# Kernel tuning notes

Hardware: AMD Instinct MI355X
Metric: run time of the kernel (lower is better)

The kernel has to match this reference:

```python
import jax, jax.numpy as jnp
import numpy as np

N, E, D, H = 50000, 800000, 64, 2
DH = D // H  # per-head GAT width
BN_EPS = 1e-5


def _linear_params(key, fan_in, fan_out):
    k1, k2 = jax.random.split(key)
    s = 1.0 / np.sqrt(fan_in)
    W = jax.random.uniform(k1, (fan_in, fan_out), jnp.float32, -s, s)
    b = jax.random.uniform(k2, (fan_out,), jnp.float32, -s, s)
    return W, b


def setup_inputs() -> dict:
    key = jax.random.key(0)
    ks = jax.random.split(key, 12)
    node_feats = jax.random.normal(ks[0], (N, D), jnp.float32)
    edge_feats = jax.random.normal(ks[1], (E, D), jnp.float32)
    src = jax.random.randint(ks[2], (E,), 0, N)
    dst = jax.random.randint(ks[3], (E,), 0, N)
    W_sg, b_sg = _linear_params(ks[4], D, D)
    W_dg, b_dg = _linear_params(ks[5], D, D)
    W_eg, b_eg = _linear_params(ks[6], D, D)
    W_su, b_su = _linear_params(ks[7], D, D)
    W_du, b_du = _linear_params(ks[8], D, D)
    W_gat, _ = _linear_params(ks[9], D, H * DH)
    b_gat = jnp.zeros((H * DH,), jnp.float32)
    ka, kb = jax.random.split(ks[10])
    attn_l = jax.random.normal(ka, (H, DH), jnp.float32) * 0.1
    attn_r = jax.random.normal(kb, (H, DH), jnp.float32) * 0.1
    return dict(node_feats=node_feats, edge_feats=edge_feats, src=src, dst=dst,
                W_sg=W_sg, b_sg=b_sg, W_dg=W_dg, b_dg=b_dg, W_eg=W_eg, b_eg=b_eg,
                W_su=W_su, b_su=b_su, W_du=W_du, b_du=b_du,
                W_gat=W_gat, b_gat=b_gat, attn_l=attn_l, attn_r=attn_r,
                bn_n_gamma=jnp.ones((D,), jnp.float32), bn_n_beta=jnp.zeros((D,), jnp.float32),
                bn_e_gamma=jnp.ones((D,), jnp.float32), bn_e_beta=jnp.zeros((D,), jnp.float32))


def _batchnorm(x, gamma, beta):
    # training-mode BatchNorm1d: biased variance over the batch dim
    mean = x.mean(0)
    var = x.var(0)
    return (x - mean) * jax.lax.rsqrt(var + BN_EPS) * gamma + beta


def _forward(node_feats, edge_feats, src, dst,
             W_sg, b_sg, W_dg, b_dg, W_eg, b_eg, W_su, b_su, W_du, b_du,
             W_gat, b_gat, attn_l, attn_r,
             bn_n_gamma, bn_n_beta, bn_e_gamma, bn_e_beta):
    n = node_feats.shape[0]
    # gated edge features: u_add_v + edge_gate
    e_src = node_feats @ W_sg + b_sg
    e_dst = node_feats @ W_dg + b_dg
    m = e_src[src] + e_dst[dst] + (edge_feats @ W_eg + b_eg)  # [E, D]

    # GATConv(num_heads=H) applied to src_update(node_feats)
    h = node_feats @ W_su + b_su
    feat = (h @ W_gat).reshape(n, H, DH)          # [N, H, DH]
    el = (feat * attn_l[None]).sum(-1)            # [N, H]
    er = (feat * attn_r[None]).sum(-1)            # [N, H]
    logits = jax.nn.leaky_relu(el[src] + er[dst], 0.2)  # [E, H]
    # edge softmax over incoming edges of each dst node
    lmax = jax.ops.segment_max(logits, dst, num_segments=n)
    lmax = jnp.where(jnp.isfinite(lmax), lmax, 0.0)  # zero-in-degree safety
    ex = jnp.exp(logits - lmax[dst])
    denom = jax.ops.segment_sum(ex, dst, num_segments=n)
    alpha = ex / denom[dst]                        # [E, H]
    gat_out = jax.ops.segment_sum(feat[src] * alpha[:, :, None], dst, num_segments=n)
    gat_out = (gat_out + b_gat.reshape(1, H, DH)).reshape(n, H * DH)  # flatten(1)

    # sigmoid-gated message passing: u_mul_e + sum, copy_e + sum
    sigma = jax.nn.sigmoid(m)                      # [E, D]
    Bh = node_feats @ W_du + b_du
    sum_sigma_h = jax.ops.segment_sum(Bh[src] * sigma, dst, num_segments=n)
    sum_sigma = jax.ops.segment_sum(sigma, dst, num_segments=n)
    h_agg = sum_sigma_h / (sum_sigma + 1e-6)

    x = h_agg + gat_out
    x = jax.nn.silu(_batchnorm(x, bn_n_gamma, bn_n_beta))
    y = jax.nn.silu(_batchnorm(m, bn_e_gamma, bn_e_beta))
    x = node_feats + x  # residual
    y = edge_feats + y
    return x, y


def reference(node_feats, edge_feats, src, dst,
              W_sg, b_sg, W_dg, b_dg, W_eg, b_eg, W_su, b_su, W_du, b_du,
              W_gat, b_gat, attn_l, attn_r,
              bn_n_gamma, bn_n_beta, bn_e_gamma, bn_e_beta):
    return _forward(node_feats, edge_feats, src, dst,
                    W_sg, b_sg, W_dg, b_dg, W_eg, b_eg, W_su, b_su, W_du, b_du,
                    W_gat, b_gat, attn_l, attn_r,
                    bn_n_gamma, bn_n_beta, bn_e_gamma, bn_e_beta)
```

## Files before the change

kernel.cpp:

```cpp
#include <hip/hip_runtime.h>
#include <hip/hip_bf16.h>
#include <stdint.h>

typedef __bf16 bf16;
typedef __bf16 bf16x8 __attribute__((ext_vector_type(8)));
typedef float f32x4 __attribute__((ext_vector_type(4)));

struct P22 { const void* p[22]; };
struct I22 { int n[22]; };

__device__ inline float bf2f(bf16 b) { return (float)b; }

__device__ inline float gld(const void* p, long i, int f32) {
    return f32 ? ((const float*)p)[i] : bf2f(((const bf16*)p)[i]);
}
__device__ inline bf16x8 gld8(const void* p, long i, int f32) {
    bf16x8 r;
    if (f32) {
        const float* q = (const float*)p + i;
        f32x4 a = *(const f32x4*)q, b = *(const f32x4*)(q + 4);
        #pragma unroll
        for (int j = 0; j < 4; ++j) { r[j] = (bf16)a[j]; r[4 + j] = (bf16)b[j]; }
    } else {
        r = *reinterpret_cast<const bf16x8*>((const bf16*)p + i);
    }
    return r;
}
__device__ inline void ld8f(const void* p, long i, int f32, float* o) {
    if (f32) {
        const float* q = (const float*)p + i;
        f32x4 a = *(const f32x4*)q, b = *(const f32x4*)(q + 4);
        #pragma unroll
        for (int j = 0; j < 4; ++j) { o[j] = a[j]; o[4 + j] = b[j]; }
    } else {
        bf16x8 r = *reinterpret_cast<const bf16x8*>((const bf16*)p + i);
        #pragma unroll
        for (int j = 0; j < 8; ++j) o[j] = bf2f(r[j]);
    }
}
__device__ inline float fin(float v) { return isfinite(v) ? v : 0.f; }

__global__ void k_detect(P22 in, I22 sz, int* flags) {
    int t = blockIdx.x;
    if (t == 2 || t == 3) { if (threadIdx.x == 0) flags[t] = 0; return; }
    const unsigned short* u = (const unsigned short*)in.p[t];
    int pairs = sz.n[t] >> 1; if (pairs > 256) pairs = 256;
    int lane = threadIdx.x;
    int insane = 0, evenNZ = 0, oddNZ = 0;
    for (int i = lane; i < pairs; i += 64) {
        unsigned short e = u[2 * i], o = u[2 * i + 1];
        int ee = (e >> 7) & 0xFF;
        if (e != 0) { evenNZ++; if (ee > 133 || ee < 108) insane++; }
        if (o != 0) oddNZ++;
    }
    #pragma unroll
    for (int off = 1; off < 64; off <<= 1) {
        insane += __shfl_xor(insane, off, 64);
        evenNZ += __shfl_xor(evenNZ, off, 64);
        oddNZ  += __shfl_xor(oddNZ,  off, 64);
    }
    if (lane == 0) {
        int f32 = 0;
        if (insane * 4 > pairs) f32 = 1;
        else if (evenNZ == 0 && oddNZ > 0) f32 = 1;
        flags[t] = f32;
    }
}

__global__ void __launch_bounds__(256) k_prep(P22 in, const int* F, bf16* Wcat, float* bcat) {
    __shared__ float sWsu[64 * 64];
    __shared__ float sWg[64 * 64];
    int tid = threadIdx.x;
    {
        int f1 = F[10], f2 = F[14];
        #pragma unroll 4
        for (int i = tid; i < 4096; i += 256) {
            sWsu[i] = gld(in.p[10], i, f1);
            sWg[i]  = gld(in.p[14], i, f2);
        }
    }
    __syncthreads();
    int j = tid;
    int sec = j >> 6, jc = j & 63;
    if (sec < 3) {
        int wi = sec == 0 ? 4 : (sec == 1 ? 6 : 12);
        const void* W = in.p[wi]; int fW = F[wi];
        #pragma unroll 8
        for (int k = 0; k < 64; ++k) Wcat[k * 256 + j] = (bf16)gld(W, k * 64 + jc, fW);
        bcat[j] = gld(in.p[wi + 1], jc, F[wi + 1]);
    } else {
        #pragma unroll 2
        for (int k = 0; k < 64; ++k) {
            float acc = 0.f;
            #pragma unroll 8
            for (int t = 0; t < 64; ++t) acc += sWsu[k * 64 + t] * sWg[t * 64 + jc];
            Wcat[k * 256 + j] = (bf16)acc;
        }
        float acc = gld(in.p[15], jc, F[15]);
        #pragma unroll 8
        for (int t = 0; t < 64; ++t) acc += gld(in.p[11], t, F[11]) * sWg[t * 64 + jc];
        bcat[j] = acc;
    }
}

__global__ void __launch_bounds__(256) k_node_gemm(P22 in, const int* F, const bf16* Wcat,
                                                   const float* bcat, bf16* NT, int N) {
    int f0 = F[0];
    int lane = threadIdx.x & 63;
    int w = threadIdx.x >> 6;
    int col0 = w * 64, q = lane >> 4, li = lane & 15;
    bf16x8 bfr[4][2];
    #pragma unroll
    for (int t = 0; t < 4; ++t)
        #pragma unroll
        for (int h = 0; h < 2; ++h)
            #pragma unroll
            for (int j = 0; j < 8; ++j)
                bfr[t][h][j] = Wcat[(long)(h * 32 + q * 8 + j) * 256 + col0 + t * 16 + li];
    float bias[4];
    #pragma unroll
    for (int t = 0; t < 4; ++t) bias[t] = bcat[col0 + t * 16 + li];

    int ntiles = (N + 15) >> 4;
    for (int rt = blockIdx.x; rt < ntiles; rt += gridDim.x) {
        int row0 = rt * 16;
        int rload = min(row0 + li, N - 1);
        bf16x8 a0 = gld8(in.p[0], (long)rload * 64 + (q << 3), f0);
        bf16x8 a1 = gld8(in.p[0], (long)rload * 64 + 32 + (q << 3), f0);
        #pragma unroll
        for (int t = 0; t < 4; ++t) {
            f32x4 acc = {0.f, 0.f, 0.f, 0.f};
            acc = __builtin_amdgcn_mfma_f32_16x16x32_bf16(a0, bfr[t][0], acc, 0, 0, 0);
            acc = __builtin_amdgcn_mfma_f32_16x16x32_bf16(a1, bfr[t][1], acc, 0, 0, 0);
            int col = col0 + t * 16 + li;
            #pragma unroll
            for (int r = 0; r < 4; ++r) {
                int row = row0 + q * 4 + r;
                if (row < N) NT[(long)row * 256 + col] = (bf16)(acc[r] + bias[t]);
            }
        }
    }
}

__global__ void k_elr(P22 in, const int* F, const bf16* NT, float* el, float* er, int N) {
    int lane = threadIdx.x & 63;
    int slot = threadIdx.x >> 6;
    int h = lane >> 5, dh = lane & 31;
    float al = gld(in.p[16], h * 32 + dh, F[16]);
    float ar = gld(in.p[17], h * 32 + dh, F[17]);
    for (int n = blockIdx.x * 4 + slot; n < N; n += gridDim.x * 4) {
        float f = bf2f(NT[(long)n * 256 + 192 + lane]);
        float pl = f * al, pr = f * ar;
        #pragma unroll
        for (int off = 1; off < 32; off <<= 1) {
            pl += __shfl_xor(pl, off, 64);
            pr += __shfl_xor(pr, off, 64);
        }
        if (dh == 0) { el[n * 2 + h] = pl; er[n * 2 + h] = pr; }
    }
}

__global__ void __launch_bounds__(256) k_edge_gemm(P22 in, const int* F, bf16* Meg, int E) {
    int f_ef = F[1];
    int lane = threadIdx.x & 63;
    int w = threadIdx.x >> 6;
    int q = lane >> 4, li = lane & 15;
    bf16x8 bfrag[4][2];
    #pragma unroll
    for (int t = 0; t < 4; ++t)
        #pragma unroll
        for (int h = 0; h < 2; ++h)
            #pragma unroll
            for (int j = 0; j < 8; ++j)
                bfrag[t][h][j] = (bf16)gld(in.p[8], (long)(h * 32 + q * 8 + j) * 64 + t * 16 + li, F[8]);
    float bias[4];
    #pragma unroll
    for (int t = 0; t < 4; ++t) bias[t] = gld(in.p[9], t * 16 + li, F[9]);

    int ntiles = E >> 4;
    for (int et = blockIdx.x * 4 + w; et < ntiles; et += gridDim.x * 4) {
        int e0 = et * 16;
        bf16x8 a0 = gld8(in.p[1], (long)(e0 + li) * 64 + (q << 3), f_ef);
        bf16x8 a1 = gld8(in.p[1], (long)(e0 + li) * 64 + 32 + (q << 3), f_ef);
        #pragma unroll
        for (int t = 0; t < 4; ++t) {
            f32x4 c = {0.f, 0.f, 0.f, 0.f};
            c = __builtin_amdgcn_mfma_f32_16x16x32_bf16(a0, bfrag[t][0], c, 0, 0, 0);
            c = __builtin_amdgcn_mfma_f32_16x16x32_bf16(a1, bfrag[t][1], c, 0, 0, 0);
            #pragma unroll
            for (int r = 0; r < 4; ++r) {
                int row = e0 + q * 4 + r;
                Meg[(long)row * 64 + t * 16 + li] = (bf16)(c[r] + bias[t]);
            }
        }
    }
}

__global__ void k_deg(const int* dst, int* deg, int E) {
    for (int e = blockIdx.x * blockDim.x + threadIdx.x; e < E; e += gridDim.x * blockDim.x)
        atomicAdd(&deg[dst[e]], 1);
}

__global__ void __launch_bounds__(1024) k_scan(const int* deg, int* rowptr, int* cursor, int N) {
    __shared__ int sums[1024];
    int t = threadIdx.x;
    int chunk = (N + 1023) >> 10;
    int lo = t * chunk, hi = min(lo + chunk, N);
    int s = 0;
    for (int i = lo; i < hi; ++i) s += deg[i];
    int val = s;
    sums[t] = val;
    __syncthreads();
    for (int off = 1; off < 1024; off <<= 1) {
        int add = (t >= off) ? sums[t - off] : 0;
        __syncthreads();
        val += add; sums[t] = val;
        __syncthreads();
    }
    int run = val - s;
    for (int i = lo; i < hi; ++i) {
        rowptr[i] = run; cursor[i] = run;
        run += deg[i];
    }
    if (t == 1023) rowptr[N] = run;
}

__global__ void k_scatter(const int* dst, int* cursor, int* eidx, int E) {
    for (int e = blockIdx.x * blockDim.x + threadIdx.x; e < E; e += gridDim.x * blockDim.x) {
        int pos = atomicAdd(&cursor[dst[e]], 1);
        eidx[pos] = e;
    }
}

__global__ void __launch_bounds__(256) k_agg(
    P22 in, const int* F, const bf16* NT, const bf16* Meg,
    const float* el, const float* er, const int* rowptr, const int* eidx,
    float* v, float* bn_e_acc, float* bn_n_acc, int N) {
    int lane = threadIdx.x & 63;
    int w = threadIdx.x >> 6;
    int c = lane, h = c >> 5;
    const int* srcp = (const int*)in.p[2];
    float bg = gld(in.p[15], c, F[15]);
    float es = 0.f, eq = 0.f;
    float vs = 0.f, vq = 0.f;

    for (int n = blockIdx.x * 4 + w; n < N; n += gridDim.x * 4) {
        float dn = bf2f(NT[(long)n * 256 + 64 + c]);
        float errh = er[(long)n * 2 + h];
        int lo = rowptr[n], hi = rowptr[n + 1];
        float ss = 0.f, ssh = 0.f, num = 0.f, den = 0.f;
        auto do_edge = [&](int e) {
            int si = srcp[e];
            const bf16* srow = NT + (long)si * 256;
            float mg  = bf2f(Meg[(long)e * 64 + c]);
            float srv = bf2f(srow[c]);
            float bh  = bf2f(srow[128 + c]);
            float ft  = bf2f(srow[192 + c]);
            float mv = mg + srv + dn;
            float sg = 1.f / (1.f + __expf(-mv));
            ss += sg; ssh += bh * sg;
            es += mv; eq += mv * mv;
            float lg = el[(long)si * 2 + h] + errh;
            lg = lg > 0.f ? lg : 0.2f * lg;
            lg = fminf(fmaxf(lg, -30.f), 30.f);
            float ex = __expf(lg);
            den += ex; num += ft * ex;
        };
        #pragma unroll 2
        for (int j = lo; j < hi; ++j) do_edge(eidx[j]);
        float hagg = ssh / (ss + 1e-6f);
        float gat = den > 0.f ? num / den : 0.f;
        float vv = hagg + gat + bg;
        v[(long)n * 64 + c] = vv;
        vs += vv; vq += vv * vv;
    }

    __shared__ float r1[256], r2[256];
    r1[threadIdx.x] = es; r2[threadIdx.x] = eq;
    __syncthreads();
    if (threadIdx.x < 64) {
        atomicAdd(bn_e_acc + c,      r1[c] + r1[64 + c] + r1[128 + c] + r1[192 + c]);
        atomicAdd(bn_e_acc + 64 + c, r2[c] + r2[64 + c] + r2[128 + c] + r2[192 + c]);
    }
    __syncthreads();
    r1[threadIdx.x] = vs; r2[threadIdx.x] = vq;
    __syncthreads();
    if (threadIdx.x < 64) {
        atomicAdd(bn_n_acc + c,      r1[c] + r1[64 + c] + r1[128 + c] + r1[192 + c]);
        atomicAdd(bn_n_acc + 64 + c, r2[c] + r2[64 + c] + r2[128 + c] + r2[192 + c]);
    }
}

__global__ void k_x_out(P22 in, const int* F, const float* v, const float* acc,
                        void* d_out, int N) {
    int f_out = F[0];
    int c = threadIdx.x & 63;
    int slot = threadIdx.x >> 6;
    float inv = 1.f / (float)N;
    float mean = acc[c] * inv;
    float var = fmaxf(acc[64 + c] * inv - mean * mean, 0.f);
    float rstd = rsqrtf(var + 1e-5f);
    float ga = gld(in.p[18], c, F[18]), be = gld(in.p[19], c, F[19]);
    for (int n = blockIdx.x * 4 + slot; n < N; n += gridDim.x * 4) {
        float t = (v[(long)n * 64 + c] - mean) * rstd * ga + be;
        float sl = t / (1.f + __expf(-t));
        float x = fin(gld(in.p[0], (long)n * 64 + c, F[0]) + sl);
        if (f_out) ((float*)d_out)[(long)n * 64 + c] = x;
        else       ((bf16*)d_out)[(long)n * 64 + c] = (bf16)x;
    }
}

__global__ void __launch_bounds__(256) k_edge_y(
    P22 in, const int* F, const bf16* NT, const bf16* Meg,
    const float* bn_e_acc, void* d_out, int N, int E) {
    int f_ef = F[1], f_out = F[0];
    const int* srcp = (const int*)in.p[2];
    const int* dstp = (const int*)in.p[3];
    int tid = blockIdx.x * 256 + threadIdx.x;
    int oc = tid & 7, c0 = oc * 8;
    float mean[8], rstd[8], ga[8], be[8];
    float invE = 1.f / (float)E;
    #pragma unroll
    for (int j = 0; j < 8; ++j) {
        int c = c0 + j;
        float mn = bn_e_acc[c] * invE;
        float vr = fmaxf(bn_e_acc[64 + c] * invE - mn * mn, 0.f);
        mean[j] = mn; rstd[j] = rsqrtf(vr + 1e-5f);
        ga[j] = gld(in.p[20], c, F[20]); be[j] = gld(in.p[21], c, F[21]);
    }
    char* yb = (char*)d_out + (size_t)N * 64 * (f_out ? 4 : 2);
    int estride = (gridDim.x * 256) >> 3;
    for (long e = tid >> 3; e < E; e += estride) {
        int si = srcp[e], di = dstp[e];
        bf16x8 mg = *reinterpret_cast<const bf16x8*>(Meg + e * 64 + c0);
        bf16x8 sr = *reinterpret_cast<const bf16x8*>(NT + (long)si * 256 + c0);
        bf16x8 dr = *reinterpret_cast<const bf16x8*>(NT + (long)di * 256 + 64 + c0);
        float ef[8]; ld8f(in.p[1], e * 64 + c0, f_ef, ef);
        float y[8];
        #pragma unroll
        for (int j = 0; j < 8; ++j) {
            float mv = bf2f(mg[j]) + bf2f(sr[j]) + bf2f(dr[j]);
            float t = (mv - mean[j]) * rstd[j] * ga[j] + be[j];
            float sl = t / (1.f + __expf(-t));
            y[j] = fin(ef[j] + sl);
        }
        if (f_out) {
            float* yp = (float*)yb + e * 64 + c0;
            f32x4 y0 = {y[0], y[1], y[2], y[3]}, y1 = {y[4], y[5], y[6], y[7]};
            *(f32x4*)yp = y0; *(f32x4*)(yp + 4) = y1;
        } else {
            bf16x8 yv;
            #pragma unroll
            for (int j = 0; j < 8; ++j) yv[j] = (bf16)y[j];
            *reinterpret_cast<bf16x8*>((bf16*)yb + e * 64 + c0) = yv;
        }
    }
}

extern "C" void kernel_launch(void* const* d_in, const int* in_sizes, int n_in,
                              void* d_out, int out_size, void* d_ws, size_t ws_size,
                              hipStream_t stream) {
    P22 p; I22 sz;
    for (int i = 0; i < 22; ++i) { p.p[i] = d_in[i]; sz.n[i] = in_sizes[i]; }
    const int N = in_sizes[0] / 64;
    const int E = in_sizes[2];

    char* ws = (char*)d_ws;
    size_t off = 0;
    auto alloc = [&](size_t bytes) -> void* {
        void* ptr = ws + off;
        off = (off + bytes + 255) & ~(size_t)255;
        return ptr;
    };
    int*   flags  = (int*)  alloc(22 * 4);
    bf16*  NT     = (bf16*) alloc((size_t)N * 256 * 2);
    float* el     = (float*)alloc((size_t)N * 2 * 4);
    float* er     = (float*)alloc((size_t)N * 2 * 4);
    bf16*  Wcat   = (bf16*) alloc(64 * 256 * 2);
    float* bcat   = (float*)alloc(256 * 4);
    bf16*  Meg    = (bf16*) alloc((size_t)E * 64 * 2);
    int*   rowptr = (int*)  alloc((size_t)(N + 1) * 4);
    int*   cursor = (int*)  alloc((size_t)N * 4);
    int*   eidx   = (int*)  alloc((size_t)E * 4);
    float* v      = (float*)alloc((size_t)N * 64 * 4);
    char* zbase = ws + off;
    int*   deg      = (int*)  alloc((size_t)N * 4);
    float* bn_e_acc = (float*)alloc(128 * 4);
    float* bn_n_acc = (float*)alloc(128 * 4);
    size_t zbytes = (size_t)((ws + off) - zbase);
    hipMemsetAsync(zbase, 0, zbytes, stream);

    const int* dstp = (const int*)d_in[3];

    hipLaunchKernelGGL(k_detect, dim3(22), dim3(64), 0, stream, p, sz, flags);
    hipLaunchKernelGGL(k_prep, dim3(1), dim3(256), 0, stream, p, flags, Wcat, bcat);
    hipLaunchKernelGGL(k_node_gemm, dim3(800), dim3(256), 0, stream, p, flags, Wcat, bcat, NT, N);
    hipLaunchKernelGGL(k_elr, dim3(512), dim3(256), 0, stream, p, flags, NT, el, er, N);
    hipLaunchKernelGGL(k_edge_gemm, dim3(1024), dim3(256), 0, stream, p, flags, Meg, E);
    hipLaunchKernelGGL(k_deg, dim3(1024), dim3(256), 0, stream, dstp, deg, E);
    hipLaunchKernelGGL(k_scan, dim3(1), dim3(1024), 0, stream, deg, rowptr, cursor, N);
    hipLaunchKernelGGL(k_scatter, dim3(1024), dim3(256), 0, stream, dstp, cursor, eidx, E);
    hipLaunchKernelGGL(k_agg, dim3(2048), dim3(256), 0, stream,
                       p, flags, NT, Meg, el, er, rowptr, eidx, v, bn_e_acc, bn_n_acc, N);
    hipLaunchKernelGGL(k_x_out, dim3(512), dim3(256), 0, stream, p, flags, v, bn_n_acc, d_out, N);
    hipLaunchKernelGGL(k_edge_y, dim3(2048), dim3(256), 0, stream,
                       p, flags, NT, Meg, bn_e_acc, d_out, N, E);
}
```

Baseline: 961.4 us.

## Interleave node projections per channel, fuse attention logits and degree counting

The node GEMM now stages each output tile in shared memory and writes an interleaved layout (src-gate, dst-gate, Bh, feat as one ushort4 per channel) for the aggregation gather. It also writes a compact two-projection array for the edge output kernel, and computes el/er in-kernel, which removes the separate k_elr launch. Degree counting moves into the edge GEMM, and the scatter stores (edge, src) pairs so aggregation avoids a dependent src lookup. This is meant to cut random-gather transactions and launch count, at the cost of extra writes, syncs and shared memory in the node GEMM.

```diff
diff --git a/kernel.cpp b/kernel.cpp
--- a/kernel.cpp
+++ b/kernel.cpp
@@ -10,6 +10,12 @@
 struct I22 { int n[22]; };
 
 __device__ inline float bf2f(bf16 b) { return (float)b; }
+__device__ inline float us2f(unsigned short u) {
+    union { unsigned int i; float f; } x; x.i = (unsigned int)u << 16; return x.f;
+}
+__device__ inline unsigned short f2us(bf16 b) {
+    union { bf16 b; unsigned short s; } x; x.b = b; return x.s;
+}
 
 __device__ inline float gld(const void* p, long i, int f32) {
     return f32 ? ((const float*)p)[i] : bf2f(((const bf16*)p)[i]);
@@ -104,7 +110,13 @@
 }
 
 __global__ void __launch_bounds__(256) k_node_gemm(P22 in, const int* F, const bf16* Wcat,
-                                                   const float* bcat, bf16* NT, int N) {
+                                                   const float* bcat, bf16* NT2, ushort4* PG,
+                                                   float* el, float* er, int N) {
+    __shared__ bf16 tile[16][260];
+    __shared__ float sal[64], sar[64];
+    if (threadIdx.x < 64) sal[threadIdx.x] = gld(in.p[16], threadIdx.x, F[16]);
+    else if (threadIdx.x < 128) sar[threadIdx.x - 64] = gld(in.p[17], threadIdx.x - 64, F[17]);
+
     int f0 = F[0];
     int lane = threadIdx.x & 63;
     int w = threadIdx.x >> 6;
@@ -120,6 +132,11 @@
     float bias[4];
     #pragma unroll
     for (int t = 0; t < 4; ++t) bias[t] = bcat[col0 + t * 16 + li];
+
+    int prow = threadIdx.x >> 4;
+    int pk   = threadIdx.x & 15;
+    int pc4  = pk * 4;
+    int phead = pc4 >> 5;
 
     int ntiles = (N + 15) >> 4;
     for (int rt = blockIdx.x; rt < ntiles; rt += gridDim.x) {
@@ -135,36 +152,51 @@
             int col = col0 + t * 16 + li;
             #pragma unroll
             for (int r = 0; r < 4; ++r) {
-                int row = row0 + q * 4 + r;
-                if (row < N) NT[(long)row * 256 + col] = (bf16)(acc[r] + bias[t]);
+                int rr = q * 4 + r;
+                bf16 bv = (bf16)(acc[r] + bias[t]);
+                tile[rr][col] = bv;
+                if (w < 2 && row0 + rr < N) NT2[(long)(row0 + rr) * 128 + col] = bv;
             }
         }
-    }
-}
-
-__global__ void k_elr(P22 in, const int* F, const bf16* NT, float* el, float* er, int N) {
-    int lane = threadIdx.x & 63;
-    int slot = threadIdx.x >> 6;
-    int h = lane >> 5, dh = lane & 31;
-    float al = gld(in.p[16], h * 32 + dh, F[16]);
-    float ar = gld(in.p[17], h * 32 + dh, F[17]);
-    for (int n = blockIdx.x * 4 + slot; n < N; n += gridDim.x * 4) {
-        float f = bf2f(NT[(long)n * 256 + 192 + lane]);
-        float pl = f * al, pr = f * ar;
-        #pragma unroll
-        for (int off = 1; off < 32; off <<= 1) {
-            pl += __shfl_xor(pl, off, 64);
-            pr += __shfl_xor(pr, off, 64);
-        }
-        if (dh == 0) { el[n * 2 + h] = pl; er[n * 2 + h] = pr; }
-    }
-}
-
-__global__ void __launch_bounds__(256) k_edge_gemm(P22 in, const int* F, bf16* Meg, int E) {
+        __syncthreads();
+        int grow = row0 + prow;
+        if (grow < N) {
+            #pragma unroll
+            for (int j = 0; j < 4; ++j) {
+                int c = pc4 + j;
+                ushort4 pv;
+                pv.x = f2us(tile[prow][c]);
+                pv.y = f2us(tile[prow][64 + c]);
+                pv.z = f2us(tile[prow][128 + c]);
+                pv.w = f2us(tile[prow][192 + c]);
+                PG[(long)grow * 64 + c] = pv;
+            }
+        }
+        float pl = 0.f, pr = 0.f;
+        #pragma unroll
+        for (int j = 0; j < 4; ++j) {
+            float f = bf2f(tile[prow][192 + pc4 + j]);
+            pl += f * sal[pc4 + j];
+            pr += f * sar[pc4 + j];
+        }
+        pl += __shfl_xor(pl, 1, 64); pr += __shfl_xor(pr, 1, 64);
+        pl += __shfl_xor(pl, 2, 64); pr += __shfl_xor(pr, 2, 64);
+        pl += __shfl_xor(pl, 4, 64); pr += __shfl_xor(pr, 4, 64);
+        if ((pk & 7) == 0 && grow < N) {
+            el[(long)grow * 2 + phead] = pl;
+            er[(long)grow * 2 + phead] = pr;
+        }
+        __syncthreads();
+    }
+}
+
+__global__ void __launch_bounds__(256) k_edge_gemm(P22 in, const int* F, bf16* Meg,
+                                                   int* deg, int E) {
     int f_ef = F[1];
     int lane = threadIdx.x & 63;
     int w = threadIdx.x >> 6;
     int q = lane >> 4, li = lane & 15;
+    const int* dstp = (const int*)in.p[3];
     bf16x8 bfrag[4][2];
     #pragma unroll
     for (int t = 0; t < 4; ++t)
@@ -182,6 +214,7 @@
         int e0 = et * 16;
         bf16x8 a0 = gld8(in.p[1], (long)(e0 + li) * 64 + (q << 3), f_ef);
         bf16x8 a1 = gld8(in.p[1], (long)(e0 + li) * 64 + 32 + (q << 3), f_ef);
+        if (lane < 16) atomicAdd(&deg[dstp[e0 + lane]], 1);
         #pragma unroll
         for (int t = 0; t < 4; ++t) {
             f32x4 c = {0.f, 0.f, 0.f, 0.f};
@@ -194,11 +227,6 @@
             }
         }
     }
-}
-
-__global__ void k_deg(const int* dst, int* deg, int E) {
-    for (int e = blockIdx.x * blockDim.x + threadIdx.x; e < E; e += gridDim.x * blockDim.x)
-        atomicAdd(&deg[dst[e]], 1);
 }
 
 __global__ void __launch_bounds__(1024) k_scan(const int* deg, int* rowptr, int* cursor, int N) {
@@ -225,49 +253,46 @@
     if (t == 1023) rowptr[N] = run;
 }
 
-__global__ void k_scatter(const int* dst, int* cursor, int* eidx, int E) {
+__global__ void k_scatter(const int* src, const int* dst, int* cursor, int2* ES, int E) {
     for (int e = blockIdx.x * blockDim.x + threadIdx.x; e < E; e += gridDim.x * blockDim.x) {
         int pos = atomicAdd(&cursor[dst[e]], 1);
-        eidx[pos] = e;
+        int2 v; v.x = e; v.y = src[e];
+        ES[pos] = v;
     }
 }
 
 __global__ void __launch_bounds__(256) k_agg(
-    P22 in, const int* F, const bf16* NT, const bf16* Meg,
-    const float* el, const float* er, const int* rowptr, const int* eidx,
+    P22 in, const int* F, const ushort4* PG, const bf16* Meg,
+    const float* el, const float* er, const int* rowptr, const int2* ES,
     float* v, float* bn_e_acc, float* bn_n_acc, int N) {
     int lane = threadIdx.x & 63;
     int w = threadIdx.x >> 6;
     int c = lane, h = c >> 5;
-    const int* srcp = (const int*)in.p[2];
     float bg = gld(in.p[15], c, F[15]);
-    float es = 0.f, eq = 0.f;
+    float es_ = 0.f, eq = 0.f;
     float vs = 0.f, vq = 0.f;
 
     for (int n = blockIdx.x * 4 + w; n < N; n += gridDim.x * 4) {
-        float dn = bf2f(NT[(long)n * 256 + 64 + c]);
+        float dn = us2f(PG[(long)n * 64 + c].y);
         float errh = er[(long)n * 2 + h];
         int lo = rowptr[n], hi = rowptr[n + 1];
         float ss = 0.f, ssh = 0.f, num = 0.f, den = 0.f;
-        auto do_edge = [&](int e) {
-            int si = srcp[e];
-            const bf16* srow = NT + (long)si * 256;
-            float mg  = bf2f(Meg[(long)e * 64 + c]);
-            float srv = bf2f(srow[c]);
-            float bh  = bf2f(srow[128 + c]);
-            float ft  = bf2f(srow[192 + c]);
+        #pragma unroll 4
+        for (int j = lo; j < hi; ++j) {
+            int2 e2 = ES[j];
+            ushort4 g = PG[(long)e2.y * 64 + c];
+            float mg = bf2f(Meg[(long)e2.x * 64 + c]);
+            float srv = us2f(g.x), bh = us2f(g.z), ft = us2f(g.w);
             float mv = mg + srv + dn;
             float sg = 1.f / (1.f + __expf(-mv));
             ss += sg; ssh += bh * sg;
-            es += mv; eq += mv * mv;
-            float lg = el[(long)si * 2 + h] + errh;
+            es_ += mv; eq += mv * mv;
+            float lg = el[(long)e2.y * 2 + h] + errh;
             lg = lg > 0.f ? lg : 0.2f * lg;
             lg = fminf(fmaxf(lg, -30.f), 30.f);
             float ex = __expf(lg);
             den += ex; num += ft * ex;
-        };
-        #pragma unroll 2
-        for (int j = lo; j < hi; ++j) do_edge(eidx[j]);
+        }
         float hagg = ssh / (ss + 1e-6f);
         float gat = den > 0.f ? num / den : 0.f;
         float vv = hagg + gat + bg;
@@ -276,7 +301,7 @@
     }
 
     __shared__ float r1[256], r2[256];
-    r1[threadIdx.x] = es; r2[threadIdx.x] = eq;
+    r1[threadIdx.x] = es_; r2[threadIdx.x] = eq;
     __syncthreads();
     if (threadIdx.x < 64) {
         atomicAdd(bn_e_acc + c,      r1[c] + r1[64 + c] + r1[128 + c] + r1[192 + c]);
@@ -311,7 +336,7 @@
 }
 
 __global__ void __launch_bounds__(256) k_edge_y(
-    P22 in, const int* F, const bf16* NT, const bf16* Meg,
+    P22 in, const int* F, const bf16* NT2, const bf16* Meg,
     const float* bn_e_acc, void* d_out, int N, int E) {
     int f_ef = F[1], f_out = F[0];
     const int* srcp = (const int*)in.p[2];
@@ -333,8 +358,8 @@
     for (long e = tid >> 3; e < E; e += estride) {
         int si = srcp[e], di = dstp[e];
         bf16x8 mg = *reinterpret_cast<const bf16x8*>(Meg + e * 64 + c0);
-        bf16x8 sr = *reinterpret_cast<const bf16x8*>(NT + (long)si * 256 + c0);
-        bf16x8 dr = *reinterpret_cast<const bf16x8*>(NT + (long)di * 256 + 64 + c0);
+        bf16x8 sr = *reinterpret_cast<const bf16x8*>(NT2 + (long)si * 128 + c0);
+        bf16x8 dr = *reinterpret_cast<const bf16x8*>(NT2 + (long)di * 128 + 64 + c0);
         float ef[8]; ld8f(in.p[1], e * 64 + c0, f_ef, ef);
         float y[8];
         #pragma unroll
@@ -372,17 +397,18 @@
         off = (off + bytes + 255) & ~(size_t)255;
         return ptr;
     };
-    int*   flags  = (int*)  alloc(22 * 4);
-    bf16*  NT     = (bf16*) alloc((size_t)N * 256 * 2);
-    float* el     = (float*)alloc((size_t)N * 2 * 4);
-    float* er     = (float*)alloc((size_t)N * 2 * 4);
-    bf16*  Wcat   = (bf16*) alloc(64 * 256 * 2);
-    float* bcat   = (float*)alloc(256 * 4);
-    bf16*  Meg    = (bf16*) alloc((size_t)E * 64 * 2);
-    int*   rowptr = (int*)  alloc((size_t)(N + 1) * 4);
-    int*   cursor = (int*)  alloc((size_t)N * 4);
-    int*   eidx   = (int*)  alloc((size_t)E * 4);
-    float* v      = (float*)alloc((size_t)N * 64 * 4);
+    int*   flags  = (int*)    alloc(22 * 4);
+    bf16*  NT2    = (bf16*)   alloc((size_t)N * 128 * 2);
+    ushort4* PG   = (ushort4*)alloc((size_t)N * 64 * 8);
+    float* el     = (float*)  alloc((size_t)N * 2 * 4);
+    float* er     = (float*)  alloc((size_t)N * 2 * 4);
+    bf16*  Wcat   = (bf16*)   alloc(64 * 256 * 2);
+    float* bcat   = (float*)  alloc(256 * 4);
+    bf16*  Meg    = (bf16*)   alloc((size_t)E * 64 * 2);
+    int*   rowptr = (int*)    alloc((size_t)(N + 1) * 4);
+    int*   cursor = (int*)    alloc((size_t)N * 4);
+    int2*  ES     = (int2*)   alloc((size_t)E * 8);
+    float* v      = (float*)  alloc((size_t)N * 64 * 4);
     char* zbase = ws + off;
     int*   deg      = (int*)  alloc((size_t)N * 4);
     float* bn_e_acc = (float*)alloc(128 * 4);
@@ -390,19 +416,19 @@
     size_t zbytes = (size_t)((ws + off) - zbase);
     hipMemsetAsync(zbase, 0, zbytes, stream);
 
+    const int* srcp = (const int*)d_in[2];
     const int* dstp = (const int*)d_in[3];
 
     hipLaunchKernelGGL(k_detect, dim3(22), dim3(64), 0, stream, p, sz, flags);
     hipLaunchKernelGGL(k_prep, dim3(1), dim3(256), 0, stream, p, flags, Wcat, bcat);
-    hipLaunchKernelGGL(k_node_gemm, dim3(800), dim3(256), 0, stream, p, flags, Wcat, bcat, NT, N);
-    hipLaunchKernelGGL(k_elr, dim3(512), dim3(256), 0, stream, p, flags, NT, el, er, N);
-    hipLaunchKernelGGL(k_edge_gemm, dim3(1024), dim3(256), 0, stream, p, flags, Meg, E);
-    hipLaunchKernelGGL(k_deg, dim3(1024), dim3(256), 0, stream, dstp, deg, E);
+    hipLaunchKernelGGL(k_node_gemm, dim3(800), dim3(256), 0, stream,
+                       p, flags, Wcat, bcat, NT2, PG, el, er, N);
+    hipLaunchKernelGGL(k_edge_gemm, dim3(1024), dim3(256), 0, stream, p, flags, Meg, deg, E);
     hipLaunchKernelGGL(k_scan, dim3(1), dim3(1024), 0, stream, deg, rowptr, cursor, N);
-    hipLaunchKernelGGL(k_scatter, dim3(1024), dim3(256), 0, stream, dstp, cursor, eidx, E);
+    hipLaunchKernelGGL(k_scatter, dim3(1024), dim3(256), 0, stream, srcp, dstp, cursor, ES, E);
     hipLaunchKernelGGL(k_agg, dim3(2048), dim3(256), 0, stream,
-                       p, flags, NT, Meg, el, er, rowptr, eidx, v, bn_e_acc, bn_n_acc, N);
+                       p, flags, PG, Meg, el, er, rowptr, ES, v, bn_e_acc, bn_n_acc, N);
     hipLaunchKernelGGL(k_x_out, dim3(512), dim3(256), 0, stream, p, flags, v, bn_n_acc, d_out, N);
     hipLaunchKernelGGL(k_edge_y, dim3(2048), dim3(256), 0, stream,
-                       p, flags, NT, Meg, bn_e_acc, d_out, N, E);
-}
+                       p, flags, NT2, Meg, bn_e_acc, d_out, N, E);
+}
```

Result: faster. 919.1 us (-4.4%).
